# Kernel tuning notes

Measured on AMD Instinct MI355X. Metric: run time of the kernel, lower is better.

Reference implementation:

```python
import jax, jax.numpy as jnp
import numpy as np

ETA = 0.1      # eta detuning in the 'experiment' dynamics
NT = 5         # integrator steps
DT = 0.5 / NT  # dt = t_end / Nt
DIM1 = 14 * 14        # 196
DIM2 = 14 * 14 + 10   # 206
BATCH = 65536


def c2q(C):
    # symmetrize, then overwrite diagonal with negative column sums
    Q = 0.5 * (C + C.T)
    d = -jnp.sum(Q, axis=0)
    n = Q.shape[0]
    idx = jnp.arange(n)
    return Q.at[idx, idx].set(d)


def ode_exp(z, Q, e, Qn):
    # 'experiment' dynamics: detuned sin + structured noise coupling Qn
    q, p = z[..., 0], z[..., 1]
    sq = jnp.sin((1.0 + ETA) * q)
    dp = -sq + e + sq @ Q + sq @ Qn
    return jnp.stack([p, dp], axis=-1)


def ode_model(z, Q, e):
    # differentiable model dynamics
    q, p = z[..., 0], z[..., 1]
    sq = jnp.sin(q)
    dp = -sq + e + sq @ Q
    return jnp.stack([p, dp], axis=-1)


def ode_map(f, z, *args):
    # explicit Euler, Nt steps (small fixed loop, unrolled)
    for _ in range(NT):
        z = z + DT * f(z, *args)
    return z


def pat(z, C, e, Qn):
    # physics-aware training: forward = experiment, gradient = model
    Q = c2q(C)
    zm = ode_map(ode_model, z, Q, e)
    ze = ode_map(lambda zz, Q_, e_: ode_exp(zz, Q_, e_, Qn), z, Q, e)
    return zm + jax.lax.stop_gradient(ze - zm)


def setup_inputs() -> dict:
    key = jax.random.key(0)
    ks = jax.random.split(key, 8)
    s1 = 1.0 / np.sqrt(DIM1)
    s2 = 1.0 / np.sqrt(DIM2)
    x = jax.random.normal(ks[0], (BATCH, DIM1), dtype=jnp.float32)
    fc1_w = jax.random.uniform(ks[1], (DIM1, DIM1), jnp.float32, -s1, s1)
    fc1_b = jax.random.uniform(ks[2], (DIM1,), jnp.float32, -s1, s1)
    fc2_w = jax.random.uniform(ks[3], (DIM2, DIM2), jnp.float32, -s2, s2)
    fc2_b = jax.random.uniform(ks[4], (DIM2,), jnp.float32, -s2, s2)
    Q_noise_small = c2q(0.2 * jax.random.normal(ks[5], (DIM1, DIM1), dtype=jnp.float32))
    Q_noise_large = c2q(0.2 * jax.random.normal(ks[6], (DIM2, DIM2), dtype=jnp.float32))
    output_fac = jnp.float32(1.0)
    return {"x": x, "fc1_w": fc1_w, "fc1_b": fc1_b, "fc2_w": fc2_w,
            "fc2_b": fc2_b, "output_fac": output_fac,
            "Q_noise_small": Q_noise_small, "Q_noise_large": Q_noise_large}


def reference(x, fc1_w, fc1_b, fc2_w, fc2_b, output_fac, Q_noise_small, Q_noise_large):
    B = x.shape[0]
    # stage 1: [B,196,2] state, PAT-integrated with fc1 weights
    z = jnp.stack([x, jnp.zeros_like(x)], axis=-1)
    z = pat(z, fc1_w, fc1_b, Q_noise_small)
    q = z[..., 0]
    # stage 2: pad with 10 class nodes -> [B,206,2]
    z = jnp.stack([q, jnp.zeros_like(q)], axis=-1)
    z = jnp.concatenate([z, jnp.zeros((B, 10, 2), dtype=x.dtype)], axis=1)
    z = pat(z, fc2_w, fc2_b, Q_noise_large)
    return output_fac * z[:, -10:, 0]
```

## Files before the change

### kernel.cpp

```cpp
#include <hip/hip_runtime.h>
#include <hip/hip_bf16.h>
#include <stdint.h>


typedef __attribute__((ext_vector_type(8))) short bh8;
typedef __attribute__((ext_vector_type(4))) float f32x4;

#define TILES 13
#define KSTEPS 7
#define ROWDW 128
#define BUFDW (16 * ROWDW)

static __device__ __forceinline__ uint16_t bf16_bits(float v) {
    __hip_bfloat16 h = __float2bfloat16(v);
    return *reinterpret_cast<uint16_t*>(&h);
}

__global__ void pack_frags(const float* __restrict__ C1, const float* __restrict__ Qn1,
                           const float* __restrict__ e1,
                           const float* __restrict__ C2, const float* __restrict__ Qn2,
                           const float* __restrict__ e2,
                           uint16_t* __restrict__ frag) {
    const int bid = blockIdx.x;
    const int st = bid / TILES, tile = bid % TILES;
    const float* C  = st ? C2 : C1;
    const float* Qn = st ? Qn2 : Qn1;
    const float* e  = st ? e2 : e1;
    const int N = st ? 206 : 196;
    const int t = threadIdx.x;
    __shared__ float part[256];
    __shared__ float dsh[16];
    {
        const int col = t & 15, seg = t >> 4;
        const int n0 = tile * 16 + col;
        float s = 0.f;
        if (n0 < N)
            for (int i = seg; i < N; i += 16)
                s += 0.5f * (C[i * N + n0] + C[n0 * N + i]);
        part[t] = s;
    }
    __syncthreads();
    if (t < 16) {
        float d = 0.f;
        #pragma unroll
        for (int j = 0; j < 16; ++j) d += part[j * 16 + t];
        dsh[t] = -d;
    }
    __syncthreads();
    const int lane = t & 63, grp = t >> 6;
    const int quad = (lane >> 4) & 3;
    const int n = tile * 16 + (lane & 15);
    for (int ks = grp; ks < KSTEPS; ks += 4) {
        uint16_t vals[8];
        #pragma unroll
        for (int j = 0; j < 8; ++j) {
            const int k = ks * 32 + quad * 8 + j;
            float v = 0.f;
            if (n < N) {
                if (k < N) {
                    if (k == n) v = dsh[lane & 15] + Qn[n * N + n] - 1.0f;
                    else        v = 0.5f * (C[k * N + n] + C[n * N + k]) + Qn[k * N + n];
                    v *= 0.1f;
                } else if (k == 208) {
                    v = 0.1f * e[n];
                }
            }
            vals[j] = bf16_bits(v);
        }
        const size_t off = ((size_t)(st * TILES + tile) * KSTEPS + ks) * 64 + lane;
        reinterpret_cast<uint4*>(frag)[off] = *reinterpret_cast<uint4*>(vals);
    }
}

__global__ __launch_bounds__(256, 3) void pat_main(
    const float* __restrict__ x, const uint16_t* __restrict__ frag,
    const float* __restrict__ fac, float* __restrict__ out) {
    __shared__ __align__(16) uint32_t sinb[3 * BUFDW];
    const int tid = threadIdx.x;
    const int lane = tid & 63;
    const int w = __builtin_amdgcn_readfirstlane(tid >> 6);
    const int c = lane & 15, quad = lane >> 4;
    const uint32_t cs = (uint32_t)(c & 7);
    const long batch = (long)blockIdx.x * 16 + c;
    const int tiles[4] = {w, w + 4, w + 8, 12};
    const int ntiles = 3 + (w == 3);

    {
        uint4 z; z.x = 0; z.y = 0; z.z = 0; z.w = 0;
        #pragma unroll
        for (int i = 0; i < 6; ++i)
            reinterpret_cast<uint4*>(sinb)[tid + i * 256] = z;
    }

    const bh8* fragv = reinterpret_cast<const bh8*>(frag);
    bh8 A[4][KSTEPS];
    #pragma unroll
    for (int nt = 0; nt < 4; ++nt)
        if (nt < ntiles)
            #pragma unroll
            for (int ks = 0; ks < KSTEPS; ++ks)
                A[nt][ks] = fragv[((size_t)tiles[nt] * KSTEPS + ks) * 64 + lane];

    float q[4][4];
    f32x4 P[4];
    #pragma unroll
    for (int nt = 0; nt < 4; ++nt) {
        const int n0 = tiles[nt] * 16 + quad * 4;
        if (nt < ntiles) {
            if (n0 + 3 < 196) {
                const float4 v = *reinterpret_cast<const float4*>(x + batch * 196 + n0);
                q[nt][0] = v.x; q[nt][1] = v.y; q[nt][2] = v.z; q[nt][3] = v.w;
            } else {
                #pragma unroll
                for (int r = 0; r < 4; ++r)
                    q[nt][r] = (n0 + r < 196) ? x[batch * 196 + n0 + r] : 0.f;
            }
        } else {
            #pragma unroll
            for (int r = 0; r < 4; ++r) q[nt][r] = 0.f;
        }
        #pragma unroll
        for (int r = 0; r < 4; ++r) P[nt][r] = 0.f;
    }
    const float fout = fac[0];

    auto sin_phase = [&](int buf) {
        #pragma unroll
        for (int nt = 0; nt < 4; ++nt)
            if (nt < ntiles) {
                uint32_t d0 = (uint32_t)bf16_bits(__sinf(1.1f * q[nt][0]))
                            | ((uint32_t)bf16_bits(__sinf(1.1f * q[nt][1])) << 16);
                uint32_t d1 = (uint32_t)bf16_bits(__sinf(1.1f * q[nt][2]))
                            | ((uint32_t)bf16_bits(__sinf(1.1f * q[nt][3])) << 16);
                const uint32_t blk = ((uint32_t)(tiles[nt] * 2 + (quad >> 1))) ^ cs;
                uint2 u; u.x = d0; u.y = d1;
                *reinterpret_cast<uint2*>(
                    &sinb[buf * BUFDW + c * ROWDW + blk * 4 + (quad & 1) * 2]) = u;
            }
    };
    auto mfma_phase = [&](int buf) {
        #pragma unroll
        for (int ks = 0; ks < KSTEPS; ++ks) {
            const bh8 b = *reinterpret_cast<const bh8*>(
                &sinb[buf * BUFDW + c * ROWDW + (((uint32_t)(ks * 4 + quad)) ^ cs) * 4]);
            #pragma unroll
            for (int nt = 0; nt < 4; ++nt)
                if (nt < ntiles)
                    P[nt] = __builtin_amdgcn_mfma_f32_16x16x32_bf16(A[nt][ks], b, P[nt], 0, 0, 0);
        }
    };
    auto q_update = [&]() {
        #pragma unroll
        for (int nt = 0; nt < 4; ++nt)
            if (nt < ntiles)
                #pragma unroll
                for (int r = 0; r < 4; ++r)
                    q[nt][r] += 0.1f * P[nt][r];
    };

    __syncthreads();
    if (tid < 48) {
        const int bb = tid >> 4, cc = tid & 15;
        sinb[bb * BUFDW + cc * ROWDW + (26u ^ (uint32_t)(cc & 7)) * 4] = 0x3F80u;
    }
    sin_phase(0);
    __syncthreads();

    for (int stg = 0; stg < 2; ++stg) {
        mfma_phase(0);
        q_update();
        sin_phase(1);
        #pragma unroll
        for (int nt = 0; nt < 4; ++nt)
            #pragma unroll
            for (int r = 0; r < 4; ++r) P[nt][r] += P[nt][r];
        q_update();
        sin_phase(2);
        __syncthreads();
        mfma_phase(1);
        q_update();
        mfma_phase(2);
        if (stg == 0) {
            #pragma unroll
            for (int nt = 0; nt < 4; ++nt)
                if (nt < ntiles)
                    #pragma unroll
                    for (int ks = 0; ks < KSTEPS; ++ks)
                        A[nt][ks] = fragv[((size_t)(TILES + tiles[nt]) * KSTEPS + ks) * 64 + lane];
        }
        q_update();
        if (stg == 0) {
            #pragma unroll
            for (int nt = 0; nt < 4; ++nt)
                #pragma unroll
                for (int r = 0; r < 4; ++r) P[nt][r] = 0.f;
            sin_phase(0);
            __syncthreads();
        }
    }

    if (w == 3) {
        const int n0 = 192 + quad * 4;
        #pragma unroll
        for (int r = 0; r < 4; ++r) {
            const int node = n0 + r;
            if (node >= 196 && node < 206)
                out[batch * 10 + (node - 196)] = fout * q[3][r];
        }
    }
}

extern "C" void kernel_launch(void* const* d_in, const int* in_sizes, int n_in,
                              void* d_out, int out_size, void* d_ws, size_t ws_size,
                              hipStream_t stream) {
    const float* x   = (const float*)d_in[0];
    const float* w1  = (const float*)d_in[1];
    const float* b1  = (const float*)d_in[2];
    const float* w2  = (const float*)d_in[3];
    const float* b2  = (const float*)d_in[4];
    const float* fac = (const float*)d_in[5];
    const float* qn1 = (const float*)d_in[6];
    const float* qn2 = (const float*)d_in[7];
    float* out = (float*)d_out;

    uint16_t* frg = (uint16_t*)d_ws;

    pack_frags<<<2 * TILES, 256, 0, stream>>>(w1, qn1, b1, w2, qn2, b2, frg);

    const int B = in_sizes[0] / 196;
    pat_main<<<B / 16, 256, 0, stream>>>(x, frg, fac, out);
}
```

Baseline: 162.3 us.

## Process two 16-row batch tiles per block to reuse A fragments

Each block now handles 32 batch rows instead of 16. The register-resident weight fragments are reused across two MFMA accumulators, which halves the per-row cost of loading fragments and doubles the independent MFMA work available to hide latency. The LDS buffers double and launch bounds drop to 2 blocks per CU, so occupancy falls. The diagonal column sums also move into a separate small kernel, which adds one launch.

```diff
diff --git a/kernel.cpp b/kernel.cpp
--- a/kernel.cpp
+++ b/kernel.cpp
@@ -9,70 +9,67 @@
 #define TILES 13
 #define KSTEPS 7
 #define ROWDW 128
-#define BUFDW (16 * ROWDW)
+#define BROWS 32
+#define BUFDW (BROWS * ROWDW)
 
 static __device__ __forceinline__ uint16_t bf16_bits(float v) {
     __hip_bfloat16 h = __float2bfloat16(v);
     return *reinterpret_cast<uint16_t*>(&h);
+}
+
+__global__ void colrow_sums(const float* __restrict__ C1,
+                            const float* __restrict__ C2,
+                            float* __restrict__ d) {
+    const float* C = blockIdx.x ? C2 : C1;
+    const int N = blockIdx.x ? 206 : 196;
+    const int j = threadIdx.x;
+    if (j >= N) { if (j < 208) d[blockIdx.x * 208 + j] = 0.f; return; }
+    float s = 0.f;
+    for (int i = 0; i < N; ++i)
+        s += C[i * N + j] + C[j * N + i];
+    d[blockIdx.x * 208 + j] = -0.5f * s;
 }
 
 __global__ void pack_frags(const float* __restrict__ C1, const float* __restrict__ Qn1,
                            const float* __restrict__ e1,
                            const float* __restrict__ C2, const float* __restrict__ Qn2,
                            const float* __restrict__ e2,
+                           const float* __restrict__ diag,
                            uint16_t* __restrict__ frag) {
     const int bid = blockIdx.x;
     const int st = bid / TILES, tile = bid % TILES;
     const float* C  = st ? C2 : C1;
     const float* Qn = st ? Qn2 : Qn1;
     const float* e  = st ? e2 : e1;
+    const float* dd = diag + st * 208;
     const int N = st ? 206 : 196;
     const int t = threadIdx.x;
-    __shared__ float part[256];
-    __shared__ float dsh[16];
-    {
-        const int col = t & 15, seg = t >> 4;
-        const int n0 = tile * 16 + col;
-        float s = 0.f;
-        if (n0 < N)
-            for (int i = seg; i < N; i += 16)
-                s += 0.5f * (C[i * N + n0] + C[n0 * N + i]);
-        part[t] = s;
-    }
-    __syncthreads();
-    if (t < 16) {
-        float d = 0.f;
-        #pragma unroll
-        for (int j = 0; j < 16; ++j) d += part[j * 16 + t];
-        dsh[t] = -d;
-    }
-    __syncthreads();
     const int lane = t & 63, grp = t >> 6;
     const int quad = (lane >> 4) & 3;
     const int n = tile * 16 + (lane & 15);
     for (int ks = grp; ks < KSTEPS; ks += 4) {
-        uint16_t vals[8];
+        union { uint16_t v16[8]; uint4 v128; } vals;
         #pragma unroll
         for (int j = 0; j < 8; ++j) {
             const int k = ks * 32 + quad * 8 + j;
             float v = 0.f;
             if (n < N) {
                 if (k < N) {
-                    if (k == n) v = dsh[lane & 15] + Qn[n * N + n] - 1.0f;
+                    if (k == n) v = dd[n] + Qn[n * N + n] - 1.0f;
                     else        v = 0.5f * (C[k * N + n] + C[n * N + k]) + Qn[k * N + n];
                     v *= 0.1f;
                 } else if (k == 208) {
                     v = 0.1f * e[n];
                 }
             }
-            vals[j] = bf16_bits(v);
+            vals.v16[j] = bf16_bits(v);
         }
         const size_t off = ((size_t)(st * TILES + tile) * KSTEPS + ks) * 64 + lane;
-        reinterpret_cast<uint4*>(frag)[off] = *reinterpret_cast<uint4*>(vals);
-    }
-}
-
-__global__ __launch_bounds__(256, 3) void pat_main(
+        reinterpret_cast<uint4*>(frag)[off] = vals.v128;
+    }
+}
+
+__global__ __launch_bounds__(256, 2) void pat_main(
     const float* __restrict__ x, const uint16_t* __restrict__ frag,
     const float* __restrict__ fac, float* __restrict__ out) {
     __shared__ __align__(16) uint32_t sinb[3 * BUFDW];
@@ -81,14 +78,14 @@
     const int w = __builtin_amdgcn_readfirstlane(tid >> 6);
     const int c = lane & 15, quad = lane >> 4;
     const uint32_t cs = (uint32_t)(c & 7);
-    const long batch = (long)blockIdx.x * 16 + c;
+    const long batch0 = (long)blockIdx.x * BROWS + c;
     const int tiles[4] = {w, w + 4, w + 8, 12};
     const int ntiles = 3 + (w == 3);
 
     {
         uint4 z; z.x = 0; z.y = 0; z.z = 0; z.w = 0;
         #pragma unroll
-        for (int i = 0; i < 6; ++i)
+        for (int i = 0; i < 12; ++i)
             reinterpret_cast<uint4*>(sinb)[tid + i * 256] = z;
     }
 
@@ -101,26 +98,31 @@
             for (int ks = 0; ks < KSTEPS; ++ks)
                 A[nt][ks] = fragv[((size_t)tiles[nt] * KSTEPS + ks) * 64 + lane];
 
-    float q[4][4];
-    f32x4 P[4];
+    float q[4][2][4];
+    f32x4 P[4][2];
     #pragma unroll
     for (int nt = 0; nt < 4; ++nt) {
         const int n0 = tiles[nt] * 16 + quad * 4;
-        if (nt < ntiles) {
-            if (n0 + 3 < 196) {
-                const float4 v = *reinterpret_cast<const float4*>(x + batch * 196 + n0);
-                q[nt][0] = v.x; q[nt][1] = v.y; q[nt][2] = v.z; q[nt][3] = v.w;
+        #pragma unroll
+        for (int bt = 0; bt < 2; ++bt) {
+            const long batch = batch0 + bt * 16;
+            if (nt < ntiles) {
+                if (n0 + 3 < 196) {
+                    const float4 v = *reinterpret_cast<const float4*>(x + batch * 196 + n0);
+                    q[nt][bt][0] = v.x; q[nt][bt][1] = v.y;
+                    q[nt][bt][2] = v.z; q[nt][bt][3] = v.w;
+                } else {
+                    #pragma unroll
+                    for (int r = 0; r < 4; ++r)
+                        q[nt][bt][r] = (n0 + r < 196) ? x[batch * 196 + n0 + r] : 0.f;
+                }
             } else {
                 #pragma unroll
-                for (int r = 0; r < 4; ++r)
-                    q[nt][r] = (n0 + r < 196) ? x[batch * 196 + n0 + r] : 0.f;
-            }
-        } else {
-            #pragma unroll
-            for (int r = 0; r < 4; ++r) q[nt][r] = 0.f;
-        }
-        #pragma unroll
-        for (int r = 0; r < 4; ++r) P[nt][r] = 0.f;
+                for (int r = 0; r < 4; ++r) q[nt][bt][r] = 0.f;
+            }
+            #pragma unroll
+            for (int r = 0; r < 4; ++r) P[nt][bt][r] = 0.f;
+        }
     }
     const float fout = fac[0];
 
@@ -128,25 +130,34 @@
         #pragma unroll
         for (int nt = 0; nt < 4; ++nt)
             if (nt < ntiles) {
-                uint32_t d0 = (uint32_t)bf16_bits(__sinf(1.1f * q[nt][0]))
-                            | ((uint32_t)bf16_bits(__sinf(1.1f * q[nt][1])) << 16);
-                uint32_t d1 = (uint32_t)bf16_bits(__sinf(1.1f * q[nt][2]))
-                            | ((uint32_t)bf16_bits(__sinf(1.1f * q[nt][3])) << 16);
                 const uint32_t blk = ((uint32_t)(tiles[nt] * 2 + (quad >> 1))) ^ cs;
-                uint2 u; u.x = d0; u.y = d1;
-                *reinterpret_cast<uint2*>(
-                    &sinb[buf * BUFDW + c * ROWDW + blk * 4 + (quad & 1) * 2]) = u;
+                #pragma unroll
+                for (int bt = 0; bt < 2; ++bt) {
+                    uint2 u;
+                    u.x = (uint32_t)bf16_bits(__sinf(1.1f * q[nt][bt][0]))
+                        | ((uint32_t)bf16_bits(__sinf(1.1f * q[nt][bt][1])) << 16);
+                    u.y = (uint32_t)bf16_bits(__sinf(1.1f * q[nt][bt][2]))
+                        | ((uint32_t)bf16_bits(__sinf(1.1f * q[nt][bt][3])) << 16);
+                    *reinterpret_cast<uint2*>(
+                        &sinb[buf * BUFDW + (c + bt * 16) * ROWDW
+                              + blk * 4 + (quad & 1) * 2]) = u;
+                }
             }
     };
     auto mfma_phase = [&](int buf) {
         #pragma unroll
         for (int ks = 0; ks < KSTEPS; ++ks) {
-            const bh8 b = *reinterpret_cast<const bh8*>(
-                &sinb[buf * BUFDW + c * ROWDW + (((uint32_t)(ks * 4 + quad)) ^ cs) * 4]);
+            const uint32_t koff = (((uint32_t)(ks * 4 + quad)) ^ cs) * 4;
+            const bh8 b0 = *reinterpret_cast<const bh8*>(
+                &sinb[buf * BUFDW + c * ROWDW + koff]);
+            const bh8 b1 = *reinterpret_cast<const bh8*>(
+                &sinb[buf * BUFDW + (c + 16) * ROWDW + koff]);
             #pragma unroll
             for (int nt = 0; nt < 4; ++nt)
-                if (nt < ntiles)
-                    P[nt] = __builtin_amdgcn_mfma_f32_16x16x32_bf16(A[nt][ks], b, P[nt], 0, 0, 0);
+                if (nt < ntiles) {
+                    P[nt][0] = __builtin_amdgcn_mfma_f32_16x16x32_bf16(A[nt][ks], b0, P[nt][0], 0, 0, 0);
+                    P[nt][1] = __builtin_amdgcn_mfma_f32_16x16x32_bf16(A[nt][ks], b1, P[nt][1], 0, 0, 0);
+                }
         }
     };
     auto q_update = [&]() {
@@ -154,13 +165,15 @@
         for (int nt = 0; nt < 4; ++nt)
             if (nt < ntiles)
                 #pragma unroll
-                for (int r = 0; r < 4; ++r)
-                    q[nt][r] += 0.1f * P[nt][r];
+                for (int bt = 0; bt < 2; ++bt)
+                    #pragma unroll
+                    for (int r = 0; r < 4; ++r)
+                        q[nt][bt][r] += 0.1f * P[nt][bt][r];
     };
 
     __syncthreads();
-    if (tid < 48) {
-        const int bb = tid >> 4, cc = tid & 15;
+    if (tid < 96) {
+        const int bb = tid >> 5, cc = tid & 31;
         sinb[bb * BUFDW + cc * ROWDW + (26u ^ (uint32_t)(cc & 7)) * 4] = 0x3F80u;
     }
     sin_phase(0);
@@ -173,7 +186,10 @@
         #pragma unroll
         for (int nt = 0; nt < 4; ++nt)
             #pragma unroll
-            for (int r = 0; r < 4; ++r) P[nt][r] += P[nt][r];
+            for (int bt = 0; bt < 2; ++bt)
+                #pragma unroll
+                for (int r = 0; r < 4; ++r)
+                    P[nt][bt][r] += P[nt][bt][r];
         q_update();
         sin_phase(2);
         __syncthreads();
@@ -193,7 +209,9 @@
             #pragma unroll
             for (int nt = 0; nt < 4; ++nt)
                 #pragma unroll
-                for (int r = 0; r < 4; ++r) P[nt][r] = 0.f;
+                for (int bt = 0; bt < 2; ++bt)
+                    #pragma unroll
+                    for (int r = 0; r < 4; ++r) P[nt][bt][r] = 0.f;
             sin_phase(0);
             __syncthreads();
         }
@@ -204,8 +222,10 @@
         #pragma unroll
         for (int r = 0; r < 4; ++r) {
             const int node = n0 + r;
-            if (node >= 196 && node < 206)
-                out[batch * 10 + (node - 196)] = fout * q[3][r];
+            if (node >= 196 && node < 206) {
+                out[batch0 * 10 + (node - 196)]        = fout * q[3][0][r];
+                out[(batch0 + 16) * 10 + (node - 196)] = fout * q[3][1][r];
+            }
         }
     }
 }
@@ -223,10 +243,12 @@
     const float* qn2 = (const float*)d_in[7];
     float* out = (float*)d_out;
 
-    uint16_t* frg = (uint16_t*)d_ws;
-
-    pack_frags<<<2 * TILES, 256, 0, stream>>>(w1, qn1, b1, w2, qn2, b2, frg);
+    float*    diag = (float*)d_ws;
+    uint16_t* frg  = (uint16_t*)((char*)d_ws + 2048);
+
+    colrow_sums<<<2, 256, 0, stream>>>(w1, w2, diag);
+    pack_frags<<<2 * TILES, 256, 0, stream>>>(w1, qn1, b1, w2, qn2, b2, diag, frg);
 
     const int B = in_sizes[0] / 196;
-    pat_main<<<B / 16, 256, 0, stream>>>(x, frg, fac, out);
-}
+    pat_main<<<B / BROWS, 256, 0, stream>>>(x, frg, fac, out);
+}
```

Result: slower. 201.4 us (+24.1%).
